# Kernel optimization log

Hardware: AMD Instinct MI355X
Metric: run time of the kernel (lower is better)

## Reference

```python
import jax, jax.numpy as jnp
import numpy as np
import math

B, L, D, H = 4, 1024, 1024, 16
HD = D // H  # head dim = 64


def setup_inputs() -> dict:
    key = jax.random.key(0)
    ks = jax.random.split(key, 8)
    s = 1.0 / math.sqrt(D)
    return {
        "Q": jax.random.normal(ks[0], (B, L, D), jnp.float32),
        "K": jax.random.normal(ks[1], (B, L, D), jnp.float32),
        "V": jax.random.normal(ks[2], (B, L, D), jnp.float32),
        "valid_lens": jax.random.randint(ks[3], (B * H * L,), 0, L, jnp.int32),
        "Wq": jax.random.normal(ks[4], (D, D), jnp.float32) * s,
        "Wk": jax.random.normal(ks[5], (D, D), jnp.float32) * s,
        "Wv": jax.random.normal(ks[6], (D, D), jnp.float32) * s,
        "Wo": jax.random.normal(ks[7], (D, D), jnp.float32) * s,
    }


def _split_heads(X):
    # [B, L, D] -> [B*H, L, HD]
    return X.reshape(B, L, H, HD).transpose(0, 2, 1, 3).reshape(B * H, L, HD)


def reference(Q, K, V, valid_lens, Wq, Wk, Wv, Wo):
    q = _split_heads(Q @ Wq.T)
    k = _split_heads(K @ Wk.T)
    v = _split_heads(V @ Wv.T)
    # scaled dot-product scores: [B*H, Lq, Lk]
    scores = jnp.einsum("bqd,bkd->bqk", q, k) / math.sqrt(HD)
    # original flattens scores to [B*H*Lq, Lk] and masks with a
    # [len(valid_lens), Lq] mask (Lq == Lk here) of -1e6, then softmax
    mask = jnp.arange(L)[None, :] < valid_lens[:, None]  # [B*H*L, L]
    flat = jnp.where(mask, scores.reshape(-1, L), jnp.float32(-1e6))
    attn = jax.nn.softmax(flat, axis=-1).reshape(B * H, L, L)
    out = jnp.einsum("bqk,bkd->bqd", attn, v)  # dropout p=0 is identity
    # merge heads: [B*H, L, HD] -> [B, L, D]
    out = out.reshape(B, H, L, HD).transpose(0, 2, 1, 3).reshape(B, L, D)
    return out @ Wo.T
```

## Files before the change

kernel.cpp:

```cpp
#include <hip/hip_runtime.h>
#include <hip/hip_bf16.h>

typedef short v8s __attribute__((ext_vector_type(8)));
typedef unsigned short v8u __attribute__((ext_vector_type(8)));
typedef float v4f __attribute__((ext_vector_type(4)));
typedef unsigned short u16;

#define LL 1024
#define DD 1024

static __device__ __forceinline__ u16 f2b(float x) {
  __hip_bfloat16 h = __float2bfloat16(x);
  return __builtin_bit_cast(u16, h);
}

static __device__ __forceinline__ void gload_lds16(const u16* g, u16* l) {
  __builtin_amdgcn_global_load_lds((const __attribute__((address_space(1))) void*)g,
                                   (__attribute__((address_space(3))) void*)l, 16, 0, 0);
}

__global__ __launch_bounds__(256) void cvt3(const float* __restrict__ p0,
                                            const float* __restrict__ p1,
                                            const float* __restrict__ p2,
                                            u16* __restrict__ out, int n8, long ostride) {
  const float* src = blockIdx.y == 0 ? p0 : (blockIdx.y == 1 ? p1 : p2);
  u16* dst = out + (long)blockIdx.y * ostride;
  int i = blockIdx.x * 256 + threadIdx.x;
  if (i >= n8) return;
  const float4* p = (const float4*)src + (long)i * 2;
  float4 a = p[0], b = p[1];
  v8u r;
  r[0] = f2b(a.x); r[1] = f2b(a.y); r[2] = f2b(a.z); r[3] = f2b(a.w);
  r[4] = f2b(b.x); r[5] = f2b(b.y); r[6] = f2b(b.z); r[7] = f2b(b.w);
  *((v8u*)dst + i) = r;
}

__global__ __launch_bounds__(256) void sortperm(const int* __restrict__ valid,
                                                u16* __restrict__ perm) {
  __shared__ int hist[1024];
  __shared__ int wsum[4];
  const int bh = blockIdx.x;
  const int tid = threadIdx.x;
  const int* v = valid + bh * 1024;
  for (int i = tid; i < 1024; i += 256) hist[i] = 0;
  __syncthreads();
  for (int i = tid; i < 1024; i += 256) {
    int k = v[i];
    k = (k == 0) ? 1023 : (k - 1);
    atomicAdd(&hist[k], 1);
  }
  __syncthreads();
  const int base = tid * 4;
  int h0 = hist[base], h1 = hist[base + 1], h2 = hist[base + 2], h3 = hist[base + 3];
  int local = h0 + h1 + h2 + h3;
  const int lane = tid & 63, w = tid >> 6;
  int scan = local;
#pragma unroll
  for (int d = 1; d < 64; d <<= 1) {
    int t = __shfl_up(scan, d);
    if (lane >= d) scan += t;
  }
  if (lane == 63) wsum[w] = scan;
  __syncthreads();
  int woff = 0;
  for (int i = 0; i < w; ++i) woff += wsum[i];
  int excl = woff + scan - local;
  hist[base] = excl;
  hist[base + 1] = excl + h0;
  hist[base + 2] = excl + h0 + h1;
  hist[base + 3] = excl + h0 + h1 + h2;
  __syncthreads();
  for (int i = tid; i < 1024; i += 256) {
    int k = v[i];
    k = (k == 0) ? 1023 : (k - 1);
    int pos = atomicAdd(&hist[k], 1);
    perm[bh * 1024 + pos] = (u16)i;
  }
}

template <typename OUTT>
__global__ __launch_bounds__(256) void gemm_bt(const u16* __restrict__ A,
                                               const u16* __restrict__ Bw,
                                               OUTT* __restrict__ C,
                                               long za, long zb, long zc) {
  __shared__ u16 As[128 * 64];
  __shared__ u16 Bs[128 * 64];
  A += (long)blockIdx.z * za;
  Bw += (long)blockIdx.z * zb;
  C += (long)blockIdx.z * zc;
  const int tid = threadIdx.x;
  const int lane = tid & 63;
  const int l15 = lane & 15, lg = lane >> 4;
  const int wid = tid >> 6;
  const int wm = wid >> 1, wn = wid & 1;
  const long mbase = (long)blockIdx.y * 128;
  const long nbase = (long)blockIdx.x * 128;

  const u16* ap = A + (mbase + (tid >> 3)) * 1024 + (tid & 7) * 8;
  const u16* bp = Bw + (nbase + (tid >> 3)) * 1024 + (tid & 7) * 8;

  v4f acc[4][4] = {};

  for (int kt = 0; kt < 16; ++kt) {
    __syncthreads();
#pragma unroll
    for (int j = 0; j < 4; ++j) {
      gload_lds16(ap + kt * 64 + j * 32 * 1024, &As[(tid + 256 * j) * 8]);
      gload_lds16(bp + kt * 64 + j * 32 * 1024, &Bs[(tid + 256 * j) * 8]);
    }
    __syncthreads();
#pragma unroll
    for (int kk = 0; kk < 2; ++kk) {
      v8s a[4], b[4];
#pragma unroll
      for (int i = 0; i < 4; ++i)
        a[i] = *(const v8s*)&As[(wm * 64 + i * 16 + l15) * 64 + kk * 32 + lg * 8];
#pragma unroll
      for (int i = 0; i < 4; ++i)
        b[i] = *(const v8s*)&Bs[(wn * 64 + i * 16 + l15) * 64 + kk * 32 + lg * 8];
#pragma unroll
      for (int mi = 0; mi < 4; ++mi)
#pragma unroll
        for (int nj = 0; nj < 4; ++nj)
          acc[mi][nj] = __builtin_amdgcn_mfma_f32_16x16x32_bf16(a[mi], b[nj], acc[mi][nj], 0, 0, 0);
    }
  }
#pragma unroll
  for (int mi = 0; mi < 4; ++mi) {
#pragma unroll
    for (int r = 0; r < 4; ++r) {
      long row = mbase + wm * 64 + mi * 16 + lg * 4 + r;
#pragma unroll
      for (int nj = 0; nj < 4; ++nj) {
        long col = nbase + wn * 64 + nj * 16 + l15;
        if constexpr (__is_same(OUTT, float))
          C[row * 1024 + col] = acc[mi][nj][r];
        else
          C[row * 1024 + col] = f2b(acc[mi][nj][r]);
      }
    }
  }
}

__global__ __launch_bounds__(256) void attn_kern(const u16* __restrict__ qb,
                                                 const u16* __restrict__ kb,
                                                 const u16* __restrict__ vb,
                                                 const int* __restrict__ valid,
                                                 const u16* __restrict__ perm,
                                                 u16* __restrict__ ob) {
  __shared__ u16 Ks[64 * 72];
  __shared__ u16 Vt[64 * 72];
  __shared__ u16 Ps[4][16 * 72];

  const int tid = threadIdx.x;
  const int lane = tid & 63;
  const int wid = tid >> 6;
  const int l15 = lane & 15, lg = lane >> 4;
  const int bh = blockIdx.y;
  const int b = bh >> 4, h = bh & 15;
  const long headoff = ((long)b * LL) * DD + h * 64;
  const u16* pblk = perm + bh * 1024 + blockIdx.x * 64;
  const u16* pp = pblk + wid * 16;

  const int qrowA = pp[l15];
  v8s qf[2];
#pragma unroll
  for (int ks = 0; ks < 2; ++ks)
    qf[ks] = *(const v8s*)(qb + headoff + (long)qrowA * DD + ks * 32 + lg * 8);

  int orow[4], vraw[4];
#pragma unroll
  for (int r = 0; r < 4; ++r) {
    int rr = pp[lg * 4 + r];
    orow[r] = rr;
    vraw[r] = valid[bh * LL + rr];
  }
  const int lastv = valid[bh * LL + pblk[63]];
  const int ntiles = ((lastv == 0 ? LL : lastv) + 63) >> 6;

  float mrow[4], lrow[4];
  v4f oacc[4] = {};
#pragma unroll
  for (int r = 0; r < 4; ++r) { mrow[r] = -1e30f; lrow[r] = 0.0f; }

  const int kk = tid & 63;
  const int qtr = tid >> 6;

  for (int kt = 0; kt < ntiles; ++kt) {
    __syncthreads();
    {
      const long rowoff = headoff + (long)(kt * 64 + kk) * DD + qtr * 16;
      v8s k0 = *(const v8s*)(kb + rowoff);
      v8s k1 = *(const v8s*)(kb + rowoff + 8);
      v8s v0 = *(const v8s*)(vb + rowoff);
      v8s v1 = *(const v8s*)(vb + rowoff + 8);
      *(v8s*)&Ks[kk * 72 + qtr * 16] = k0;
      *(v8s*)&Ks[kk * 72 + qtr * 16 + 8] = k1;
      v8u u0 = __builtin_bit_cast(v8u, v0);
      v8u u1 = __builtin_bit_cast(v8u, v1);
#pragma unroll
      for (int j = 0; j < 8; ++j) Vt[(qtr * 16 + j) * 72 + kk] = u0[j];
#pragma unroll
      for (int j = 0; j < 8; ++j) Vt[(qtr * 16 + 8 + j) * 72 + kk] = u1[j];
    }
    __syncthreads();

    v4f s[4];
    __builtin_amdgcn_s_setprio(1);
#pragma unroll
    for (int t = 0; t < 4; ++t) {
      v4f z = {};
#pragma unroll
      for (int ks = 0; ks < 2; ++ks) {
        v8s kf = *(const v8s*)&Ks[(t * 16 + l15) * 72 + ks * 32 + lg * 8];
        z = __builtin_amdgcn_mfma_f32_16x16x32_bf16(qf[ks], kf, z, 0, 0, 0);
      }
      s[t] = z;
    }
    __builtin_amdgcn_s_setprio(0);

    const int colbase = kt * 64 + l15;
#pragma unroll
    for (int t = 0; t < 4; ++t)
#pragma unroll
      for (int r = 0; r < 4; ++r) {
        float val = s[t][r] * 0.125f;
        s[t][r] = (colbase + t * 16 < vraw[r]) ? val : -1e6f;
      }

    float pm[4];
#pragma unroll
    for (int r = 0; r < 4; ++r)
      pm[r] = fmaxf(fmaxf(s[0][r], s[1][r]), fmaxf(s[2][r], s[3][r]));
#pragma unroll
    for (int d = 1; d < 16; d <<= 1)
#pragma unroll
      for (int r = 0; r < 4; ++r) pm[r] = fmaxf(pm[r], __shfl_xor(pm[r], d));

    bool sk = true;
#pragma unroll
    for (int r = 0; r < 4; ++r) sk = sk && (pm[r] <= mrow[r] + 8.0f);
    if (!__all(sk)) {
#pragma unroll
      for (int r = 0; r < 4; ++r) {
        float mn = fmaxf(mrow[r], pm[r]);
        float sc = __expf(mrow[r] - mn);
        mrow[r] = mn;
        lrow[r] *= sc;
#pragma unroll
        for (int t = 0; t < 4; ++t) oacc[t][r] *= sc;
      }
    }
    float rs[4] = {0.f, 0.f, 0.f, 0.f};
#pragma unroll
    for (int t = 0; t < 4; ++t)
#pragma unroll
      for (int r = 0; r < 4; ++r) {
        float p = __expf(s[t][r] - mrow[r]);
        s[t][r] = p;
        rs[r] += p;
      }
#pragma unroll
    for (int d = 1; d < 16; d <<= 1)
#pragma unroll
      for (int r = 0; r < 4; ++r) rs[r] += __shfl_xor(rs[r], d);
#pragma unroll
    for (int r = 0; r < 4; ++r) lrow[r] += rs[r];

#pragma unroll
    for (int t = 0; t < 4; ++t)
#pragma unroll
      for (int r = 0; r < 4; ++r)
        Ps[wid][(lg * 4 + r) * 72 + t * 16 + l15] = f2b(s[t][r]);

    asm volatile("s_waitcnt lgkmcnt(0)" ::: "memory");
    __builtin_amdgcn_sched_barrier(0);

    __builtin_amdgcn_s_setprio(1);
#pragma unroll
    for (int ks = 0; ks < 2; ++ks) {
      v8s pa = *(const v8s*)&Ps[wid][l15 * 72 + ks * 32 + lg * 8];
#pragma unroll
      for (int t = 0; t < 4; ++t) {
        v8s vf = *(const v8s*)&Vt[(t * 16 + l15) * 72 + ks * 32 + lg * 8];
        oacc[t] = __builtin_amdgcn_mfma_f32_16x16x32_bf16(pa, vf, oacc[t], 0, 0, 0);
      }
    }
    __builtin_amdgcn_s_setprio(0);
  }

#pragma unroll
  for (int r = 0; r < 4; ++r) {
    float inv = 1.0f / lrow[r];
    long rp = headoff + (long)orow[r] * DD;
#pragma unroll
    for (int t = 0; t < 4; ++t)
      ob[rp + t * 16 + l15] = f2b(oacc[t][r] * inv);
  }
}

extern "C" void kernel_launch(void* const* d_in, const int* in_sizes, int n_in,
                              void* d_out, int out_size, void* d_ws, size_t ws_size,
                              hipStream_t stream) {
  const float* Q = (const float*)d_in[0];
  const float* K = (const float*)d_in[1];
  const float* V = (const float*)d_in[2];
  const int* valid = (const int*)d_in[3];
  const float* Wq = (const float*)d_in[4];
  const float* Wk = (const float*)d_in[5];
  const float* Wv = (const float*)d_in[6];
  const float* Wo = (const float*)d_in[7];
  float* out = (float*)d_out;

  u16* ws = (u16*)d_ws;
  const long MK = 4096L * 1024;
  const long NK = 1024L * 1024;
  u16* qkvb = ws;
  u16* wqkv = qkvb + 3 * MK;
  u16* wo = wqkv + 3 * NK;
  u16* proj = wo + NK;
  u16* ob = proj + 3 * MK;
  u16* perm = qkvb;

  cvt3<<<dim3(2048, 3), 256, 0, stream>>>(Q, K, V, qkvb, (int)(MK / 8), MK);
  cvt3<<<dim3(512, 3), 256, 0, stream>>>(Wq, Wk, Wv, wqkv, (int)(NK / 8), NK);
  cvt3<<<dim3(512, 1), 256, 0, stream>>>(Wo, Wo, Wo, wo, (int)(NK / 8), 0);

  gemm_bt<u16><<<dim3(8, 32, 3), 256, 0, stream>>>(qkvb, wqkv, proj, MK, NK, MK);
  sortperm<<<64, 256, 0, stream>>>(valid, perm);
  attn_kern<<<dim3(16, 64), 256, 0, stream>>>(proj, proj + MK, proj + 2 * MK, valid, perm, ob);
  gemm_bt<float><<<dim3(8, 32, 1), 256, 0, stream>>>(ob, wo, out, 0, 0, 0);
}
```

Measured before the change: 156.2 us.

## Prefetch next K/V tile into registers, use exp2 softmax, reverse block order

Loads the next K/V tile into registers while the current tile is processed, so global load latency overlaps with the MFMA and softmax work. Softmax now works in base 2: scores are prescaled by log2(e)/8 and exp2 replaces __expf, with the lazy-rescale threshold moved from 8 to 11 to match. Query blocks are taken in reverse order so the heavier blocks (sorted by valid length) launch first, which should balance the tail. Register pressure rises because of the extra staged vectors.

```diff
diff --git a/kernel.cpp b/kernel.cpp
--- a/kernel.cpp
+++ b/kernel.cpp
@@ -159,7 +159,8 @@
   const int bh = blockIdx.y;
   const int b = bh >> 4, h = bh & 15;
   const long headoff = ((long)b * LL) * DD + h * 64;
-  const u16* pblk = perm + bh * 1024 + blockIdx.x * 64;
+  const int gq = 15 - (int)blockIdx.x;
+  const u16* pblk = perm + bh * 1024 + gq * 64;
   const u16* pp = pblk + wid * 16;
 
   const int qrowA = pp[l15];
@@ -185,24 +186,33 @@
 
   const int kk = tid & 63;
   const int qtr = tid >> 6;
+  const long stagebase = headoff + (long)kk * DD + qtr * 16;
+
+  v8s rk0 = *(const v8s*)(kb + stagebase);
+  v8s rk1 = *(const v8s*)(kb + stagebase + 8);
+  v8s rv0 = *(const v8s*)(vb + stagebase);
+  v8s rv1 = *(const v8s*)(vb + stagebase + 8);
 
   for (int kt = 0; kt < ntiles; ++kt) {
     __syncthreads();
+    *(v8s*)&Ks[kk * 72 + qtr * 16] = rk0;
+    *(v8s*)&Ks[kk * 72 + qtr * 16 + 8] = rk1;
     {
-      const long rowoff = headoff + (long)(kt * 64 + kk) * DD + qtr * 16;
-      v8s k0 = *(const v8s*)(kb + rowoff);
-      v8s k1 = *(const v8s*)(kb + rowoff + 8);
-      v8s v0 = *(const v8s*)(vb + rowoff);
-      v8s v1 = *(const v8s*)(vb + rowoff + 8);
-      *(v8s*)&Ks[kk * 72 + qtr * 16] = k0;
-      *(v8s*)&Ks[kk * 72 + qtr * 16 + 8] = k1;
-      v8u u0 = __builtin_bit_cast(v8u, v0);
-      v8u u1 = __builtin_bit_cast(v8u, v1);
+      v8u u0 = __builtin_bit_cast(v8u, rv0);
+      v8u u1 = __builtin_bit_cast(v8u, rv1);
 #pragma unroll
       for (int j = 0; j < 8; ++j) Vt[(qtr * 16 + j) * 72 + kk] = u0[j];
 #pragma unroll
       for (int j = 0; j < 8; ++j) Vt[(qtr * 16 + 8 + j) * 72 + kk] = u1[j];
     }
+    if (kt + 1 < ntiles) {
+      const long noff = stagebase + (long)(kt + 1) * 64 * DD;
+      rk0 = *(const v8s*)(kb + noff);
+      rk1 = *(const v8s*)(kb + noff + 8);
+      rv0 = *(const v8s*)(vb + noff);
+      rv1 = *(const v8s*)(vb + noff + 8);
+    }
+    __builtin_amdgcn_sched_barrier(0);
     __syncthreads();
 
     v4f s[4];
@@ -219,12 +229,13 @@
     }
     __builtin_amdgcn_s_setprio(0);
 
+    const float SC = 0.18033688f;
     const int colbase = kt * 64 + l15;
 #pragma unroll
     for (int t = 0; t < 4; ++t)
 #pragma unroll
       for (int r = 0; r < 4; ++r) {
-        float val = s[t][r] * 0.125f;
+        float val = s[t][r] * SC;
         s[t][r] = (colbase + t * 16 < vraw[r]) ? val : -1e6f;
       }
 
@@ -239,12 +250,12 @@
 
     bool sk = true;
 #pragma unroll
-    for (int r = 0; r < 4; ++r) sk = sk && (pm[r] <= mrow[r] + 8.0f);
+    for (int r = 0; r < 4; ++r) sk = sk && (pm[r] <= mrow[r] + 11.0f);
     if (!__all(sk)) {
 #pragma unroll
       for (int r = 0; r < 4; ++r) {
         float mn = fmaxf(mrow[r], pm[r]);
-        float sc = __expf(mrow[r] - mn);
+        float sc = __builtin_amdgcn_exp2f(mrow[r] - mn);
         mrow[r] = mn;
         lrow[r] *= sc;
 #pragma unroll
@@ -256,7 +267,7 @@
     for (int t = 0; t < 4; ++t)
 #pragma unroll
       for (int r = 0; r < 4; ++r) {
-        float p = __expf(s[t][r] - mrow[r]);
+        float p = __builtin_amdgcn_exp2f(s[t][r] - mrow[r]);
         s[t][r] = p;
         rs[r] += p;
       }
```

After: 154.5 us. About the same (-1.1%).
